# Optimization experiments

Measured on AMD Instinct MI355X. Metric: run time of the kernel, lower is better.

## Reference

```python
import jax, jax.numpy as jnp
import numpy as np

B, N, D = 2, 2048, 2048
H = 16
HD = D // H          # 128
R = 512              # kv_rank
INT4_MIN, INT4_MAX = -8, 7


def setup_inputs() -> dict:
    key = jax.random.key(0)
    ks = jax.random.split(key, 6)
    sD = 1.0 / np.sqrt(D)
    sR = 1.0 / np.sqrt(R)
    return {
        "x":   jax.random.normal(ks[0], (B, N, D), dtype=jnp.float32),
        "Wq":  jax.random.normal(ks[1], (D, D), dtype=jnp.float32) * sD,
        "bq":  jnp.zeros((D,), dtype=jnp.float32),
        "Wkv": jax.random.normal(ks[2], (D, R), dtype=jnp.float32) * sD,
        "bkv": jnp.zeros((R,), dtype=jnp.float32),
        "Wku": jax.random.normal(ks[3], (R, D), dtype=jnp.float32) * sR,
        "bku": jnp.zeros((D,), dtype=jnp.float32),
        "Wvu": jax.random.normal(ks[4], (R, D), dtype=jnp.float32) * sR,
        "bvu": jnp.zeros((D,), dtype=jnp.float32),
        "Wo":  jax.random.normal(ks[5], (D, D), dtype=jnp.float32) * sD * 0.1,
        "bo":  jnp.zeros((D,), dtype=jnp.float32),
    }


def _int4_quant_dequant(t):
    # per_channel=True, 3D tensor: amax over dims [0,1], keepdim
    amax = jnp.max(jnp.abs(t), axis=(0, 1), keepdims=True)
    amax = jnp.maximum(amax, 1e-5)
    scale = (amax / 7.0).astype(jnp.float32)
    q = jnp.clip(jnp.round(t / scale), INT4_MIN, INT4_MAX).astype(jnp.int8)
    return q.astype(jnp.float32) * scale


def reference(x, Wq, bq, Wkv, bkv, Wku, bku, Wvu, bvu, Wo, bo):
    q = x @ Wq + bq                              # (B,N,D)
    kv_latent = x @ Wkv + bkv                    # (B,N,R)
    kv_latent = _int4_quant_dequant(kv_latent)   # use_cache=True path
    k = kv_latent @ Wku + bku                    # (B,N,D)
    v = kv_latent @ Wvu + bvu                    # (B,N,D)

    q4 = q.reshape(B, N, H, HD)
    k4 = k.reshape(B, N, H, HD)
    v4 = v.reshape(B, N, H, HD)

    attn = jnp.einsum("bqhd,bkhd->bhqk", q4, k4) * (HD ** -0.5)
    attn = jax.nn.softmax(attn.astype(jnp.float32), axis=-1).astype(x.dtype)
    out = jnp.einsum("bhqk,bkhd->bqhd", attn, v4).reshape(B, N, D)
    return out @ Wo + bo
```

## Files before the change

### kernel.cpp

```cpp
#include <hip/hip_runtime.h>
#include <stdint.h>

typedef __attribute__((ext_vector_type(8))) _Float16 half8;
typedef __attribute__((ext_vector_type(4))) _Float16 half4;
typedef __attribute__((ext_vector_type(4))) float f32x4;

#define AS1 __attribute__((address_space(1)))
#define AS3 __attribute__((address_space(3)))

__device__ inline void gload_lds16(const void* g, void* l) {
  __builtin_amdgcn_global_load_lds((const AS1 void*)g, (AS3 void*)l, 16, 0, 0);
}
__device__ inline f32x4 mfma16h(half8 a, half8 b, f32x4 c) {
  return __builtin_amdgcn_mfma_f32_16x16x32_f16(a, b, c, 0, 0, 0);
}

__global__ __launch_bounds__(256) void cvt_split(const float4* __restrict__ in,
                                                 half4* __restrict__ xh,
                                                 half4* __restrict__ xl, int nq) {
  int i = blockIdx.x * 256 + threadIdx.x;
  if (i >= nq) return;
  float4 v = in[i];
  float vv[4] = {v.x, v.y, v.z, v.w};
  half4 h, lo;
#pragma unroll
  for (int j = 0; j < 4; ++j) {
    _Float16 hh = (_Float16)vv[j];
    h[j] = hh;
    lo[j] = (_Float16)((vv[j] - (float)hh) * 4096.0f);
  }
  xh[i] = h;
  xl[i] = lo;
}

__global__ __launch_bounds__(256) void transpose_f16(const float* __restrict__ in,
                                                     const float* __restrict__ in2,
                                                     _Float16* __restrict__ outh,
                                                     _Float16* __restrict__ outl,
                                                     const float* __restrict__ rowamax,
                                                     int R, int C) {
  __shared__ float t[32][33];
  if (blockIdx.z) { in = in2; outh += (size_t)R * C; }
  const int tx = threadIdx.x, ty = threadIdx.y;
  const int r0 = blockIdx.y * 32, c0 = blockIdx.x * 32;
#pragma unroll
  for (int k = 0; k < 4; ++k) {
    const int r = r0 + ty + k * 8;
    float s = 1.0f;
    if (rowamax) s = fmaxf(rowamax[r], 1e-5f) / 7.0f;
    t[ty + k * 8][tx] = in[(size_t)r * C + c0 + tx] * s;
  }
  __syncthreads();
#pragma unroll
  for (int k = 0; k < 4; ++k) {
    const int c = c0 + ty + k * 8;
    float v = t[tx][ty + k * 8];
    _Float16 h = (_Float16)v;
    outh[(size_t)c * R + r0 + tx] = h;
    if (outl) outl[(size_t)c * R + r0 + tx] = (_Float16)((v - (float)h) * 4096.0f);
  }
}

__global__ __launch_bounds__(256) void gemm_kv16(const _Float16* __restrict__ Ah,
                                                 const _Float16* __restrict__ Al,
                                                 const _Float16* __restrict__ Bh,
                                                 const _Float16* __restrict__ Bl,
                                                 const float* __restrict__ bias,
                                                 float* __restrict__ C,
                                                 float* __restrict__ amax,
                                                 int M, int N, int K) {
  __shared__ _Float16 sAh[128 * 64], sAl[128 * 64];
  __shared__ _Float16 sBh[64 * 64], sBl[64 * 64];
  const int tid = threadIdx.x;
  const int w = tid >> 6, l = tid & 63, g = l >> 4, c = l & 15;
  const int wr = w >> 1, wc = w & 1;
  const int tm0 = blockIdx.y * 128, n0 = blockIdx.x * 64;

  f32x4 acc[4][2], acc2[4][2];
#pragma unroll
  for (int i = 0; i < 4; ++i)
#pragma unroll
    for (int j = 0; j < 2; ++j) {
      acc[i][j] = f32x4{0.f, 0.f, 0.f, 0.f};
      acc2[i][j] = f32x4{0.f, 0.f, 0.f, 0.f};
    }

  for (int k0 = 0; k0 < K; k0 += 64) {
#pragma unroll
    for (int cc = 0; cc < 4; ++cc) {
      const int off = w * 4096 + cc * 1024 + l * 16;
      const int row = off >> 7, colb = off & 127;
      const char* gA = (const char*)Ah + ((size_t)(tm0 + row) * K + k0) * 2 + colb;
      const char* gL = (const char*)Al + ((size_t)(tm0 + row) * K + k0) * 2 + colb;
      gload_lds16(gA, (char*)sAh + w * 4096 + cc * 1024);
      gload_lds16(gL, (char*)sAl + w * 4096 + cc * 1024);
    }
#pragma unroll
    for (int cc = 0; cc < 2; ++cc) {
      const int off = w * 2048 + cc * 1024 + l * 16;
      const int row = off >> 7, colb = off & 127;
      const char* gB = (const char*)Bh + ((size_t)(n0 + row) * K + k0) * 2 + colb;
      const char* gL = (const char*)Bl + ((size_t)(n0 + row) * K + k0) * 2 + colb;
      gload_lds16(gB, (char*)sBh + w * 2048 + cc * 1024);
      gload_lds16(gL, (char*)sBl + w * 2048 + cc * 1024);
    }
    __syncthreads();
#pragma unroll
    for (int ks = 0; ks < 2; ++ks) {
      half8 ah[4], al[4], bh[2], bl[2];
#pragma unroll
      for (int i = 0; i < 4; ++i) {
        ah[i] = *(const half8*)&sAh[(wr * 64 + i * 16 + c) * 64 + ks * 32 + g * 8];
        al[i] = *(const half8*)&sAl[(wr * 64 + i * 16 + c) * 64 + ks * 32 + g * 8];
      }
#pragma unroll
      for (int j = 0; j < 2; ++j) {
        bh[j] = *(const half8*)&sBh[(wc * 32 + j * 16 + c) * 64 + ks * 32 + g * 8];
        bl[j] = *(const half8*)&sBl[(wc * 32 + j * 16 + c) * 64 + ks * 32 + g * 8];
      }
#pragma unroll
      for (int i = 0; i < 4; ++i)
#pragma unroll
        for (int j = 0; j < 2; ++j) {
          acc[i][j] = mfma16h(ah[i], bh[j], acc[i][j]);
          acc2[i][j] = mfma16h(al[i], bh[j], acc2[i][j]);
          acc2[i][j] = mfma16h(ah[i], bl[j], acc2[i][j]);
        }
    }
    __syncthreads();
  }

  float cm[2] = {0.f, 0.f};
#pragma unroll
  for (int i = 0; i < 4; ++i) {
    const int row0 = tm0 + wr * 64 + i * 16 + g * 4;
#pragma unroll
    for (int j = 0; j < 2; ++j) {
      const int col = n0 + wc * 32 + j * 16 + c;
      const float bv = bias[col];
#pragma unroll
      for (int r = 0; r < 4; ++r) {
        float v = acc[i][j][r] + acc2[i][j][r] * 2.44140625e-4f + bv;
        C[(size_t)(row0 + r) * N + col] = v;
        cm[j] = fmaxf(cm[j], fabsf(v));
      }
    }
  }
#pragma unroll
  for (int j = 0; j < 2; ++j) {
    float m = cm[j];
    m = fmaxf(m, __shfl_xor(m, 16, 64));
    m = fmaxf(m, __shfl_xor(m, 32, 64));
    if (g == 0) atomicMax((int*)amax + (n0 + wc * 32 + j * 16 + c), __float_as_int(m));
  }
}

__global__ __launch_bounds__(256) void quant_kernel(const float4* __restrict__ kv,
                                                    const float* __restrict__ amax,
                                                    half4* __restrict__ kvq, int nq) {
  int i = blockIdx.x * 256 + threadIdx.x;
  if (i >= nq) return;
  float4 v = kv[i];
  int r0 = (i * 4) & 511;
  half4 o;
#pragma unroll
  for (int j = 0; j < 4; ++j) {
    float s = fmaxf(amax[r0 + j], 1e-5f) / 7.0f;
    float val = (j == 0) ? v.x : (j == 1) ? v.y : (j == 2) ? v.z : v.w;
    float q = rintf(val / s);
    q = fminf(7.f, fmaxf(-8.f, q));
    o[j] = (_Float16)q;
  }
  kvq[i] = o;
}

template <int MODE>
__global__ __launch_bounds__(256) void gemm_bt(const _Float16* __restrict__ A,
                                               const _Float16* __restrict__ BT,
                                               void* __restrict__ Cout,
                                               void* __restrict__ Cout2,
                                               const float* __restrict__ bias,
                                               const float* __restrict__ bias2,
                                               float cscale,
                                               int M, int N, int K) {
  __shared__ _Float16 As[128 * 64];
  __shared__ _Float16 Bs[128 * 64];
  const int tid = threadIdx.x;
  const int w = tid >> 6, l = tid & 63, g = l >> 4, c = l & 15;
  const int wr = w >> 1, wc = w & 1;
  const int tm0 = blockIdx.y * 128, tn0 = blockIdx.x * 128;

  f32x4 acc[4][4];
#pragma unroll
  for (int i = 0; i < 4; ++i)
#pragma unroll
    for (int j = 0; j < 4; ++j) acc[i][j] = f32x4{0.f, 0.f, 0.f, 0.f};

  for (int k0 = 0; k0 < K; k0 += 64) {
#pragma unroll
    for (int cc = 0; cc < 4; ++cc) {
      const int off = w * 4096 + cc * 1024 + l * 16;
      const int row = off >> 7, colb = off & 127;
      const char* gA = (const char*)A + ((size_t)(tm0 + row) * K + k0) * 2 + colb;
      const char* gB = (const char*)BT + ((size_t)(tn0 + row) * K + k0) * 2 + colb;
      gload_lds16(gA, (char*)As + w * 4096 + cc * 1024);
      gload_lds16(gB, (char*)Bs + w * 4096 + cc * 1024);
    }
    __syncthreads();
#pragma unroll
    for (int ks = 0; ks < 2; ++ks) {
      half8 a[4], b[4];
#pragma unroll
      for (int i = 0; i < 4; ++i)
        a[i] = *(const half8*)&As[(wr * 64 + i * 16 + c) * 64 + ks * 32 + g * 8];
#pragma unroll
      for (int j = 0; j < 4; ++j)
        b[j] = *(const half8*)&Bs[(wc * 64 + j * 16 + c) * 64 + ks * 32 + g * 8];
#pragma unroll
      for (int i = 0; i < 4; ++i)
#pragma unroll
        for (int j = 0; j < 4; ++j) acc[i][j] = mfma16h(a[i], b[j], acc[i][j]);
    }
    __syncthreads();
  }

#pragma unroll
  for (int i = 0; i < 4; ++i) {
    const int row0 = tm0 + wr * 64 + i * 16 + g * 4;
#pragma unroll
    for (int j = 0; j < 4; ++j) {
      const int col = tn0 + wc * 64 + j * 16 + c;
      if constexpr (MODE == 0) {
        const float bv = bias[col];
#pragma unroll
        for (int r = 0; r < 4; ++r)
          ((_Float16*)Cout)[(size_t)(row0 + r) * N + col] =
              (_Float16)((acc[i][j][r] + bv) * cscale);
      } else if constexpr (MODE == 4) {
        const int bI = row0 >> 11;
        const int colk = col & 2047;
        const int hI = colk >> 7, dI = colk & 127;
        if (col < 2048) {
          const float bv = bias[colk];
#pragma unroll
          for (int r = 0; r < 4; ++r) {
            const int n = (row0 + r) & 2047;
            ((_Float16*)Cout)[(size_t)((bI * 16 + hI) * 32 + (n >> 6)) * 8192 +
                              (n & 63) * 128 + dI] = (_Float16)(acc[i][j][r] + bv);
          }
        } else {
          const float bv = bias2[colk];
          half4 pk;
#pragma unroll
          for (int r = 0; r < 4; ++r) pk[r] = (_Float16)(acc[i][j][r] + bv);
          const int nI = row0 & 2047;
          *(half4*)((_Float16*)Cout2 +
                    (size_t)((bI * 16 + hI) * 32 + (nI >> 6)) * 8192 + dI * 64 + (nI & 63)) = pk;
        }
      } else {
        const float bv = bias[col];
#pragma unroll
        for (int r = 0; r < 4; ++r)
          ((float*)Cout)[(size_t)(row0 + r) * N + col] = acc[i][j][r] + bv;
      }
    }
  }
}

__global__ __launch_bounds__(512, 4) void flash_attn(const _Float16* __restrict__ Q,
                                                     const _Float16* __restrict__ KB,
                                                     const _Float16* __restrict__ VB,
                                                     _Float16* __restrict__ O) {
  __shared__ _Float16 Ks[2][8192];
  __shared__ _Float16 Vs[2][8192];
  __shared__ _Float16 Ps[8][1024];
  const int tid = threadIdx.x, w = tid >> 6, l = tid & 63, g = l >> 4, c = l & 15;
  const int wgid = blockIdx.x + blockIdx.y * 16;
  const int xcd = wgid & 7, idx = wgid >> 3;
  const int bh = xcd * 4 + (idx >> 4), qblk = idx & 15;
  const int b = bh >> 4, h = bh & 15;
  const size_t rowQ0 = (size_t)b * 2048 + qblk * 128 + w * 16;
  const _Float16* kvK = KB + (size_t)bh * 262144;
  const _Float16* kvV = VB + (size_t)bh * 262144;
  const int sxc = (c & 7) ^ ((c >> 1) & 6);

  auto stageK = [&](int t, int buf) {
#pragma unroll
    for (int i = 0; i < 2; ++i) {
      const int o = i * 8192 + tid * 16;
      const int row = o >> 8;
      const int src = (o & ~255) | ((o & 255) ^ ((row & 7) << 4));
      gload_lds16((const char*)(kvK + t * 8192) + src,
                  (char*)&Ks[buf][0] + i * 8192 + w * 1024);
    }
  };
  auto stageV = [&](int t, int buf) {
#pragma unroll
    for (int i = 0; i < 2; ++i) {
      const int o = i * 8192 + tid * 16;
      const int row = o >> 7;
      const int src = (o & ~127) | ((o & 127) ^ ((row & 7) << 4));
      gload_lds16((const char*)(kvV + t * 8192) + src,
                  (char*)&Vs[buf][0] + i * 8192 + w * 1024);
    }
  };

  stageK(0, 0);
  stageV(0, 0);
  half8 aq[4];
#pragma unroll
  for (int ks = 0; ks < 4; ++ks)
    aq[ks] = *(const half8*)&Q[(rowQ0 + c) * 2048 + h * 128 + ks * 32 + g * 8];

  f32x4 accO[8];
#pragma unroll
  for (int n = 0; n < 8; ++n) accO[n] = f32x4{0.f, 0.f, 0.f, 0.f};
  float lsum[4] = {0.f, 0.f, 0.f, 0.f};

  __syncthreads();

  for (int t = 0; t < 32; ++t) {
    const int cur = t & 1;
    if (t < 31) { stageK(t + 1, cur ^ 1); stageV(t + 1, cur ^ 1); }
    f32x4 accS[4];
#pragma unroll
    for (int n = 0; n < 4; ++n) accS[n] = f32x4{0.f, 0.f, 0.f, 0.f};
    __builtin_amdgcn_s_setprio(1);
#pragma unroll
    for (int ks = 0; ks < 4; ++ks) {
      half8 bk[4];
#pragma unroll
      for (int n = 0; n < 4; ++n) {
        const int row = n * 16 + c;
        bk[n] = *(const half8*)((const char*)&Ks[cur][0] + row * 256 +
                                ((ks * 64 + g * 16) ^ ((c & 7) << 4)));
      }
#pragma unroll
      for (int n = 0; n < 4; ++n) accS[n] = mfma16h(aq[ks], bk[n], accS[n]);
    }
    __builtin_amdgcn_s_setprio(0);
#pragma unroll
    for (int n = 0; n < 4; ++n)
#pragma unroll
      for (int r = 0; r < 4; ++r) {
        const float p = __expf(accS[n][r]);
        lsum[r] += p;
        const int row = g * 4 + r;
        const int sxw = ((row & 7) ^ ((row >> 1) & 6));
        *(_Float16*)((char*)&Ps[w][0] + row * 128 +
                     ((n * 32 + c * 2) ^ (sxw << 4))) = (_Float16)p;
      }
    __builtin_amdgcn_s_setprio(1);
#pragma unroll
    for (int ks = 0; ks < 2; ++ks) {
      half8 ap = *(const half8*)((const char*)&Ps[w][0] + c * 128 +
                                 ((ks * 64 + g * 16) ^ (sxc << 4)));
#pragma unroll
      for (int n = 0; n < 8; ++n) {
        const int vrow = n * 16 + c;
        half8 bv = *(const half8*)((const char*)&Vs[cur][0] + vrow * 128 +
                                   ((ks * 64 + g * 16) ^ ((c & 7) << 4)));
        accO[n] = mfma16h(ap, bv, accO[n]);
      }
    }
    __builtin_amdgcn_s_setprio(0);
    __syncthreads();
  }

#pragma unroll
  for (int r = 0; r < 4; ++r) {
    float ps = lsum[r];
#pragma unroll
    for (int off = 1; off < 16; off <<= 1) ps += __shfl_xor(ps, off, 64);
    const float inv = 1.f / ps;
#pragma unroll
    for (int n = 0; n < 8; ++n) {
      float v = accO[n][r] * inv;
      O[(rowQ0 + g * 4 + r) * 2048 + h * 128 + n * 16 + c] = (_Float16)v;
    }
  }
}

#define SCALE_QK 0.08838834764831845f

extern "C" void kernel_launch(void* const* d_in, const int* in_sizes, int n_in,
                              void* d_out, int out_size, void* d_ws, size_t ws_size,
                              hipStream_t stream) {
  const float* x   = (const float*)d_in[0];
  const float* Wq  = (const float*)d_in[1];
  const float* bq  = (const float*)d_in[2];
  const float* Wkv = (const float*)d_in[3];
  const float* bkv = (const float*)d_in[4];
  const float* Wku = (const float*)d_in[5];
  const float* bku = (const float*)d_in[6];
  const float* Wvu = (const float*)d_in[7];
  const float* bvu = (const float*)d_in[8];
  const float* Wo  = (const float*)d_in[9];
  const float* bo  = (const float*)d_in[10];
  float* out = (float*)d_out;

  char* ws = (char*)d_ws;
  const size_t MB = 1ull << 20;
  _Float16* xh   = (_Float16*)(ws + 0 * MB);
  _Float16* attn = (_Float16*)(ws + 0 * MB);
  _Float16* xl   = (_Float16*)(ws + 16 * MB);
  _Float16* qb   = (_Float16*)(ws + 16 * MB);
  _Float16* kb   = (_Float16*)(ws + 32 * MB);
  _Float16* vT   = (_Float16*)(ws + 48 * MB);
  _Float16* WqT  = (_Float16*)(ws + 64 * MB);
  _Float16* WoT  = (_Float16*)(ws + 72 * MB);
  float* kv      = (float*)(ws + 80 * MB);
  _Float16* kvq  = (_Float16*)(ws + 88 * MB);
  _Float16* WkvTh = (_Float16*)(ws + 92 * MB);
  _Float16* WkvTl = (_Float16*)(ws + 94 * MB);
  _Float16* WkuT = (_Float16*)(ws + 96 * MB);
  _Float16* WvuT = (_Float16*)(ws + 98 * MB);
  float* amax    = (float*)(ws + 100 * MB);

  hipMemsetAsync(amax, 0, 512 * sizeof(float), stream);

  cvt_split<<<8192, 256, 0, stream>>>((const float4*)x, (half4*)xh, (half4*)xl, 2097152);
  transpose_f16<<<dim3(64, 64, 2), dim3(32, 8), 0, stream>>>(Wq, Wo, WqT, nullptr, nullptr, 2048, 2048);
  transpose_f16<<<dim3(16, 64), dim3(32, 8), 0, stream>>>(Wkv, nullptr, WkvTh, WkvTl, nullptr, 2048, 512);
  gemm_kv16<<<dim3(8, 32), 256, 0, stream>>>(xh, xl, WkvTh, WkvTl, bkv, kv, amax, 4096, 512, 2048);
  quant_kernel<<<2048, 256, 0, stream>>>((const float4*)kv, amax, (half4*)kvq, 524288);
  transpose_f16<<<dim3(64, 16, 2), dim3(32, 8), 0, stream>>>(Wku, Wvu, WkuT, nullptr, amax, 512, 2048);
  gemm_bt<0><<<dim3(16, 32), 256, 0, stream>>>(xh, WqT, qb, nullptr, bq, nullptr, SCALE_QK,
                                               4096, 2048, 2048);
  gemm_bt<4><<<dim3(32, 32), 256, 0, stream>>>(kvq, WkuT, kb, vT, bku, bvu, 1.0f,
                                               4096, 4096, 512);
  flash_attn<<<dim3(16, 32), 512, 0, stream>>>(qb, kb, vT, attn);
  gemm_bt<2><<<dim3(16, 32), 256, 0, stream>>>(attn, WoT, out, nullptr, bo, nullptr, 1.0f,
                                               4096, 2048, 2048);

  (void)in_sizes; (void)n_in; (void)out_size; (void)ws_size;
}
```

Baseline: 337.9 us.

## Split flash attention KV tile across wave groups and read V directly from global

```diff
diff --git a/kernel.cpp b/kernel.cpp
--- a/kernel.cpp
+++ b/kernel.cpp
@@ -272,17 +272,16 @@
                                                      const _Float16* __restrict__ VB,
                                                      _Float16* __restrict__ O) {
   __shared__ _Float16 Ks[2][8192];
-  __shared__ _Float16 Vs[2][8192];
   __shared__ _Float16 Ps[8][1024];
   const int tid = threadIdx.x, w = tid >> 6, l = tid & 63, g = l >> 4, c = l & 15;
+  const int hk = w >> 2, wq = w & 3;
   const int wgid = blockIdx.x + blockIdx.y * 16;
   const int xcd = wgid & 7, idx = wgid >> 3;
   const int bh = xcd * 4 + (idx >> 4), qblk = idx & 15;
   const int b = bh >> 4, h = bh & 15;
-  const size_t rowQ0 = (size_t)b * 2048 + qblk * 128 + w * 16;
+  const size_t rowQ0 = (size_t)b * 2048 + qblk * 128 + wq * 32;
   const _Float16* kvK = KB + (size_t)bh * 262144;
   const _Float16* kvV = VB + (size_t)bh * 262144;
-  const int sxc = (c & 7) ^ ((c >> 1) & 6);
 
   auto stageK = [&](int t, int buf) {
 #pragma unroll
@@ -294,90 +293,124 @@
                   (char*)&Ks[buf][0] + i * 8192 + w * 1024);
     }
   };
-  auto stageV = [&](int t, int buf) {
-#pragma unroll
-    for (int i = 0; i < 2; ++i) {
-      const int o = i * 8192 + tid * 16;
-      const int row = o >> 7;
-      const int src = (o & ~127) | ((o & 127) ^ ((row & 7) << 4));
-      gload_lds16((const char*)(kvV + t * 8192) + src,
-                  (char*)&Vs[buf][0] + i * 8192 + w * 1024);
-    }
-  };
 
   stageK(0, 0);
-  stageV(0, 0);
-  half8 aq[4];
-#pragma unroll
-  for (int ks = 0; ks < 4; ++ks)
-    aq[ks] = *(const half8*)&Q[(rowQ0 + c) * 2048 + h * 128 + ks * 32 + g * 8];
-
-  f32x4 accO[8];
-#pragma unroll
-  for (int n = 0; n < 8; ++n) accO[n] = f32x4{0.f, 0.f, 0.f, 0.f};
-  float lsum[4] = {0.f, 0.f, 0.f, 0.f};
+  half8 aq[2][4];
+#pragma unroll
+  for (int m = 0; m < 2; ++m)
+#pragma unroll
+    for (int ks = 0; ks < 4; ++ks)
+      aq[m][ks] = *(const half8*)&Q[(rowQ0 + m * 16 + c) * 2048 + h * 128 + ks * 32 + g * 8];
+
+  f32x4 accO[2][8];
+#pragma unroll
+  for (int m = 0; m < 2; ++m)
+#pragma unroll
+    for (int n = 0; n < 8; ++n) accO[m][n] = f32x4{0.f, 0.f, 0.f, 0.f};
+  float lsum[2][4];
+#pragma unroll
+  for (int m = 0; m < 2; ++m)
+#pragma unroll
+    for (int r = 0; r < 4; ++r) lsum[m][r] = 0.f;
 
   __syncthreads();
 
   for (int t = 0; t < 32; ++t) {
     const int cur = t & 1;
-    if (t < 31) { stageK(t + 1, cur ^ 1); stageV(t + 1, cur ^ 1); }
-    f32x4 accS[4];
-#pragma unroll
-    for (int n = 0; n < 4; ++n) accS[n] = f32x4{0.f, 0.f, 0.f, 0.f};
+    if (t < 31) stageK(t + 1, cur ^ 1);
+#pragma unroll
+    for (int n = 0; n < 2; ++n) {
+      f32x4 s0 = f32x4{0.f, 0.f, 0.f, 0.f};
+      f32x4 s1 = f32x4{0.f, 0.f, 0.f, 0.f};
+      __builtin_amdgcn_s_setprio(1);
+#pragma unroll
+      for (int ks = 0; ks < 4; ++ks) {
+        const int row = hk * 32 + n * 16 + c;
+        half8 bk = *(const half8*)((const char*)&Ks[cur][0] + row * 256 +
+                                   ((ks * 64 + g * 16) ^ ((c & 7) << 4)));
+        s0 = mfma16h(aq[0][ks], bk, s0);
+        s1 = mfma16h(aq[1][ks], bk, s1);
+      }
+      __builtin_amdgcn_s_setprio(0);
+#pragma unroll
+      for (int m = 0; m < 2; ++m)
+#pragma unroll
+        for (int r = 0; r < 4; ++r) {
+          const float p = __expf(m == 0 ? s0[r] : s1[r]);
+          lsum[m][r] += p;
+          const int row = m * 16 + g * 4 + r;
+          *(_Float16*)((char*)&Ps[w][0] + row * 64 +
+                       ((n * 32 + c * 2) ^ (r << 4))) = (_Float16)p;
+        }
+    }
+    half8 ap[2];
+#pragma unroll
+    for (int m = 0; m < 2; ++m)
+      ap[m] = *(const half8*)((const char*)&Ps[w][0] + (m * 16 + c) * 64 +
+                              ((g * 16) ^ ((c & 3) << 4)));
     __builtin_amdgcn_s_setprio(1);
 #pragma unroll
-    for (int ks = 0; ks < 4; ++ks) {
-      half8 bk[4];
-#pragma unroll
-      for (int n = 0; n < 4; ++n) {
-        const int row = n * 16 + c;
-        bk[n] = *(const half8*)((const char*)&Ks[cur][0] + row * 256 +
-                                ((ks * 64 + g * 16) ^ ((c & 7) << 4)));
-      }
-#pragma unroll
-      for (int n = 0; n < 4; ++n) accS[n] = mfma16h(aq[ks], bk[n], accS[n]);
-    }
-    __builtin_amdgcn_s_setprio(0);
-#pragma unroll
-    for (int n = 0; n < 4; ++n)
-#pragma unroll
-      for (int r = 0; r < 4; ++r) {
-        const float p = __expf(accS[n][r]);
-        lsum[r] += p;
-        const int row = g * 4 + r;
-        const int sxw = ((row & 7) ^ ((row >> 1) & 6));
-        *(_Float16*)((char*)&Ps[w][0] + row * 128 +
-                     ((n * 32 + c * 2) ^ (sxw << 4))) = (_Float16)p;
-      }
-    __builtin_amdgcn_s_setprio(1);
-#pragma unroll
-    for (int ks = 0; ks < 2; ++ks) {
-      half8 ap = *(const half8*)((const char*)&Ps[w][0] + c * 128 +
-                                 ((ks * 64 + g * 16) ^ (sxc << 4)));
-#pragma unroll
-      for (int n = 0; n < 8; ++n) {
-        const int vrow = n * 16 + c;
-        half8 bv = *(const half8*)((const char*)&Vs[cur][0] + vrow * 128 +
-                                   ((ks * 64 + g * 16) ^ ((c & 7) << 4)));
-        accO[n] = mfma16h(ap, bv, accO[n]);
-      }
+    for (int n = 0; n < 8; ++n) {
+      half8 bv = *(const half8*)(kvV + (size_t)t * 8192 + (n * 16 + c) * 64 +
+                                 hk * 32 + g * 8);
+      accO[0][n] = mfma16h(ap[0], bv, accO[0][n]);
+      accO[1][n] = mfma16h(ap[1], bv, accO[1][n]);
     }
     __builtin_amdgcn_s_setprio(0);
     __syncthreads();
   }
 
-#pragma unroll
-  for (int r = 0; r < 4; ++r) {
-    float ps = lsum[r];
-#pragma unroll
-    for (int off = 1; off < 16; off <<= 1) ps += __shfl_xor(ps, off, 64);
-    const float inv = 1.f / ps;
-#pragma unroll
-    for (int n = 0; n < 8; ++n) {
-      float v = accO[n][r] * inv;
-      O[(rowQ0 + g * 4 + r) * 2048 + h * 128 + n * 16 + c] = (_Float16)v;
-    }
+  float* redO = (float*)&Ks[0][0];
+  float* redL = (float*)&Ps[0][0];
+  const int pr = w & 3;
+  if (hk == 1) {
+#pragma unroll
+    for (int m = 0; m < 2; ++m)
+#pragma unroll
+      for (int r = 0; r < 4; ++r) redL[(pr * 64 + l) * 8 + m * 4 + r] = lsum[m][r];
+#pragma unroll
+    for (int n = 0; n < 8; ++n)
+#pragma unroll
+      for (int r = 0; r < 4; ++r) redO[(pr * 64 + l) * 32 + n * 4 + r] = accO[0][n][r];
+  }
+  __syncthreads();
+  if (hk == 0) {
+#pragma unroll
+    for (int m = 0; m < 2; ++m)
+#pragma unroll
+      for (int r = 0; r < 4; ++r) lsum[m][r] += redL[(pr * 64 + l) * 8 + m * 4 + r];
+#pragma unroll
+    for (int n = 0; n < 8; ++n)
+#pragma unroll
+      for (int r = 0; r < 4; ++r) accO[0][n][r] += redO[(pr * 64 + l) * 32 + n * 4 + r];
+  }
+  __syncthreads();
+  if (hk == 1) {
+#pragma unroll
+    for (int n = 0; n < 8; ++n)
+#pragma unroll
+      for (int r = 0; r < 4; ++r) redO[(pr * 64 + l) * 32 + n * 4 + r] = accO[1][n][r];
+  }
+  __syncthreads();
+  if (hk == 0) {
+#pragma unroll
+    for (int n = 0; n < 8; ++n)
+#pragma unroll
+      for (int r = 0; r < 4; ++r) accO[1][n][r] += redO[(pr * 64 + l) * 32 + n * 4 + r];
+#pragma unroll
+    for (int m = 0; m < 2; ++m)
+#pragma unroll
+      for (int r = 0; r < 4; ++r) {
+        float ps = lsum[m][r];
+#pragma unroll
+        for (int off = 1; off < 16; off <<= 1) ps += __shfl_xor(ps, off, 64);
+        const float inv = 1.f / ps;
+#pragma unroll
+        for (int n = 0; n < 8; ++n) {
+          float v = accO[m][n][r] * inv;
+          O[(rowQ0 + m * 16 + g * 4 + r) * 2048 + h * 128 + n * 16 + c] = (_Float16)v;
+        }
+      }
   }
 }
 
```

Result: slower. 471.2 us (+39.5%).
